# Kernel optimization log

Hardware: AMD Instinct MI355X
Metric: run time of the kernel (lower is better)

## Reference

```python
import jax, jax.numpy as jnp
import numpy as np

D_MODEL = 1024
NUM_HEADS = 16
D_HEAD = D_MODEL // NUM_HEADS
THETA = 10000.0


def _apply_rope(x, pos):
    # x: [B, H, S, Dh]; pos: [S]
    inv_freq = 1.0 / (THETA ** (jnp.arange(0, D_HEAD, 2, dtype=jnp.float32) / D_HEAD))  # [Dh/2]
    freqs = pos[:, None].astype(x.dtype) * inv_freq.astype(x.dtype)  # [S, Dh/2]
    cos = jnp.cos(freqs)  # [S, Dh/2]
    sin = jnp.sin(freqs)
    x1 = x[..., 0::2]  # [B, H, S, Dh/2]
    x2 = x[..., 1::2]
    even = x1 * cos - x2 * sin
    odd = x1 * sin + x2 * cos
    # interleave back: stack on last axis then flatten
    out = jnp.stack([even, odd], axis=-1).reshape(x.shape)
    return out


def setup_inputs() -> dict:
    key = jax.random.key(0)
    k0, k1, k2, k3, k4 = jax.random.split(key, 5)
    B, S = 2, 2048
    scale = 0.02
    return {
        "in_features": jax.random.normal(k0, (B, S, D_MODEL), dtype=jnp.float32),
        "Wq": jax.random.normal(k1, (D_MODEL, D_MODEL), dtype=jnp.float32) * scale,
        "Wk": jax.random.normal(k2, (D_MODEL, D_MODEL), dtype=jnp.float32) * scale,
        "Wv": jax.random.normal(k3, (D_MODEL, D_MODEL), dtype=jnp.float32) * scale,
        "Wo": jax.random.normal(k4, (D_MODEL, D_MODEL), dtype=jnp.float32) * scale,
    }


def reference(in_features, Wq, Wk, Wv, Wo):
    B, S, _ = in_features.shape
    H, Dh = NUM_HEADS, D_HEAD

    def proj(W):
        # torch Linear: y = x @ W^T; split heads -> [B, H, S, Dh]
        y = jnp.einsum('bsd,ed->bse', in_features, W)
        return y.reshape(B, S, H, Dh).transpose(0, 2, 1, 3)

    q = proj(Wq)
    k = proj(Wk)
    v = proj(Wv)

    pos = jnp.arange(S)
    q = _apply_rope(q, pos)
    k = _apply_rope(k, pos)

    scores = jnp.einsum('bhqd,bhkd->bhqk', q, k) / jnp.sqrt(jnp.asarray(Dh, q.dtype))
    causal = jnp.tril(jnp.ones((S, S), dtype=bool))  # True = keep
    scores = jnp.where(causal[None, None, :, :], scores, -jnp.inf)
    att = jax.nn.softmax(scores, axis=-1)
    out = jnp.einsum('bhqk,bhkd->bhqd', att, v)  # [B, H, S, Dh]
    out = out.transpose(0, 2, 1, 3).reshape(B, S, H * Dh)
    return jnp.einsum('bsd,ed->bse', out, Wo)
```

## Files before the change

kernel.cpp:

```cpp
#include <hip/hip_runtime.h>
#include <hip/hip_bf16.h>
#include <math.h>

#define D_MODEL 1024
#define NHEAD 16
#define DHEAD 64
#define SEQ 2048
#define BATCH 2
#define MTOT (BATCH * SEQ)

typedef __attribute__((ext_vector_type(8))) short bf16x8;
typedef __attribute__((ext_vector_type(4))) float f32x4;

static __device__ __forceinline__ ushort f2b(float x) {
  __hip_bfloat16 h = __float2bfloat16(x);
  union { __hip_bfloat16 h; ushort u; } cv; cv.h = h; return cv.u;
}

#define GLLDS16(gp, lp)                                                     \
  __builtin_amdgcn_global_load_lds(                                         \
      (const __attribute__((address_space(1))) unsigned int*)(gp),          \
      (__attribute__((address_space(3))) unsigned int*)(lp), 16, 0, 0)

#define QSCALE 0.18033688011112042f

__global__ __launch_bounds__(256)
void prep(const float* __restrict__ X, const float* __restrict__ Wq,
          const float* __restrict__ Wk, const float* __restrict__ Wv,
          const float* __restrict__ Wo, ushort* __restrict__ Xb,
          ushort* __restrict__ Wqb, ushort* __restrict__ Wkb,
          ushort* __restrict__ Wvb, ushort* __restrict__ Wob,
          float2* __restrict__ tbl) {
  int bid = blockIdx.x;
  if (bid >= 8192) {
    int idx = (bid - 8192) * 256 + threadIdx.x;
    int s = idx >> 5, i = idx & 31;
    float inv = exp2f((float)i * -0.4152410118609203f);
    float sn, cs;
    sincosf((float)s * inv, &sn, &cs);
    tbl[idx] = make_float2(cs, sn);
    return;
  }
  const float* in;
  ushort* out;
  int i;
  if (bid < 4096) {
    in = X; out = Xb; i = bid * 256 + threadIdx.x;
  } else {
    int ws = (bid - 4096) >> 10;
    in = (ws == 0) ? Wq : (ws == 1) ? Wk : (ws == 2) ? Wv : Wo;
    out = (ws == 0) ? Wqb : (ws == 1) ? Wkb : (ws == 2) ? Wvb : Wob;
    i = ((bid - 4096) & 1023) * 256 + threadIdx.x;
  }
  float4 v = ((const float4*)in)[i];
  ushort4 o;
  o.x = f2b(v.x); o.y = f2b(v.y); o.z = f2b(v.z); o.w = f2b(v.w);
  ((ushort4*)out)[i] = o;
}

__global__ __launch_bounds__(256)
void gemm_bf16(const ushort* __restrict__ A,
               const ushort* __restrict__ W0, const ushort* __restrict__ W1,
               const ushort* __restrict__ W2,
               const float2* __restrict__ tbl,
               float* __restrict__ outF,
               ushort* __restrict__ o0, ushort* __restrict__ o1,
               ushort* __restrict__ o2, int mode) {
  __shared__ ushort As[128 * 32];
  __shared__ ushort Bs[128 * 32];
  const int tid = threadIdx.x;
  const int lane = tid & 63;
  const int w = tid >> 6;
  const int quad = lane >> 4, l15 = lane & 15;
  const int wy = w >> 1, wx = w & 1;
  const int m0 = blockIdx.y * 128, n0 = blockIdx.x * 128;
  const int z = blockIdx.z;
  const ushort* W = (z == 0) ? W0 : (z == 1) ? W1 : W2;
  ushort* outB = (z == 0) ? o0 : (z == 1) ? o1 : o2;

  const int r0 = tid >> 2, c0 = tid & 3;
  const int gc = c0 ^ (((r0 >> 2) ^ r0) & 3);
  const ushort* Ag0 = A + (size_t)(m0 + r0) * D_MODEL + gc * 8;
  const ushort* Ag1 = A + (size_t)(m0 + r0 + 64) * D_MODEL + gc * 8;
  const ushort* Wg0 = W + (size_t)(n0 + r0) * D_MODEL + gc * 8;
  const ushort* Wg1 = W + (size_t)(n0 + r0 + 64) * D_MODEL + gc * 8;

  const int sw = (quad ^ (l15 >> 2) ^ l15) & 3;

  f32x4 acc[4][4];
#pragma unroll
  for (int i = 0; i < 4; ++i)
#pragma unroll
    for (int j = 0; j < 4; ++j) acc[i][j] = (f32x4){0.f, 0.f, 0.f, 0.f};

  for (int kt = 0; kt < D_MODEL / 32; ++kt) {
    if (kt) __syncthreads();
    GLLDS16(Ag0 + kt * 32, &As[(size_t)tid * 8]);
    GLLDS16(Ag1 + kt * 32, &As[(size_t)(tid + 256) * 8]);
    GLLDS16(Wg0 + kt * 32, &Bs[(size_t)tid * 8]);
    GLLDS16(Wg1 + kt * 32, &Bs[(size_t)(tid + 256) * 8]);
    __syncthreads();

    bf16x8 af[4], bfr[4];
#pragma unroll
    for (int mt = 0; mt < 4; ++mt) {
      int row = wy * 64 + mt * 16 + l15;
      af[mt] = *(const bf16x8*)&As[(row * 4 + sw) * 8];
    }
#pragma unroll
    for (int nt = 0; nt < 4; ++nt) {
      int row = wx * 64 + nt * 16 + l15;
      bfr[nt] = *(const bf16x8*)&Bs[(row * 4 + sw) * 8];
    }
#pragma unroll
    for (int mt = 0; mt < 4; ++mt)
#pragma unroll
      for (int nt = 0; nt < 4; ++nt)
        acc[mt][nt] = __builtin_amdgcn_mfma_f32_16x16x32_bf16(
            af[mt], bfr[nt], acc[mt][nt], 0, 0, 0);
  }

  const float qsc = (z == 0) ? QSCALE : 1.0f;
#pragma unroll
  for (int mt = 0; mt < 4; ++mt) {
    int m_base = m0 + wy * 64 + mt * 16 + quad * 4;
    int b = m_base >> 11, s_base = m_base & (SEQ - 1);
#pragma unroll
    for (int nt = 0; nt < 4; ++nt) {
      int n = n0 + wx * 64 + nt * 16 + l15;
      if (mode == 0) {
#pragma unroll
        for (int r = 0; r < 4; ++r)
          outF[(size_t)(m_base + r) * D_MODEL + n] = acc[mt][nt][r];
      } else {
        int h = n >> 6, dh = n & 63;
        if (z == 2) {
          ushort4 o;
          o.x = f2b(acc[mt][nt][0]); o.y = f2b(acc[mt][nt][1]);
          o.z = f2b(acc[mt][nt][2]); o.w = f2b(acc[mt][nt][3]);
          *(ushort4*)&outB[((size_t)(b * NHEAD + h) * DHEAD + dh) * SEQ + s_base] = o;
        } else {
          int i = nt * 8 + (l15 >> 1);
          bool evn = !(l15 & 1);
#pragma unroll
          for (int r = 0; r < 4; ++r) {
            float v = acc[mt][nt][r];
            float pv = __shfl_xor(v, 1);
            float2 csn = tbl[(s_base + r) * 32 + i];
            v = v * csn.x + (evn ? -pv * csn.y : pv * csn.y);
            v *= qsc;
            outB[(((size_t)(b * NHEAD + h)) * SEQ + s_base + r) * DHEAD + dh] = f2b(v);
          }
        }
      }
    }
  }
}

__global__ __launch_bounds__(256)
void flash_mfma(const ushort* __restrict__ Q, const ushort* __restrict__ K,
                const ushort* __restrict__ Vt, ushort* __restrict__ O) {
  __shared__ ushort Ks[64 * 64];
  __shared__ ushort Vs[64 * 64];
  __shared__ ushort Ps[4][16][68];
  const int tid = threadIdx.x;
  const int lane = tid & 63, w = tid >> 6;
  const int quad = lane >> 4, l15 = lane & 15;
  const int h = blockIdx.y, b = blockIdx.z;
  const int qt = (h >= 8) ? (31 - blockIdx.x) : blockIdx.x;
  const int bh = b * NHEAD + h;

  const ushort* Qrow = Q + ((size_t)bh * SEQ + qt * 64 + w * 16 + l15) * 64;
  bf16x8 aq0 = *(const bf16x8*)(Qrow + quad * 8);
  bf16x8 aq1 = *(const bf16x8*)(Qrow + 32 + quad * 8);

  const int rl = tid >> 3;
  const int gsc = (tid & 7) ^ (rl & 7);
  const ushort* Kg  = K  + ((size_t)bh * SEQ + rl) * 64 + gsc * 8;
  const ushort* Kg2 = Kg + (size_t)32 * 64;
  const ushort* Vg  = Vt + ((size_t)bh * 64 + rl) * SEQ + gsc * 8;
  const ushort* Vg2 = Vg + (size_t)32 * SEQ;

  const int sA = (quad ^ (l15 & 7)) * 8;
  const int sB = sA ^ 32;

  float rsl[4];
  f32x4 accO[4];
#pragma unroll
  for (int r = 0; r < 4; ++r) rsl[r] = 0.f;
#pragma unroll
  for (int nt = 0; nt < 4; ++nt) accO[nt] = (f32x4){0.f, 0.f, 0.f, 0.f};

  const int qrow0 = qt * 64 + w * 16 + quad * 4;

  for (int kt = 0; kt <= qt; ++kt) {
    __syncthreads();
    GLLDS16(Kg  + (size_t)kt * 64 * 64, &Ks[tid * 8]);
    GLLDS16(Kg2 + (size_t)kt * 64 * 64, &Ks[2048 + tid * 8]);
    GLLDS16(Vg  + kt * 64,              &Vs[tid * 8]);
    GLLDS16(Vg2 + kt * 64,              &Vs[2048 + tid * 8]);
    __syncthreads();

    f32x4 sc[4];
#pragma unroll
    for (int nt = 0; nt < 4; ++nt) {
      const ushort* kr = &Ks[(nt * 16 + l15) * 64];
      bf16x8 bk0 = *(const bf16x8*)(kr + sA);
      bf16x8 bk1 = *(const bf16x8*)(kr + sB);
      f32x4 zz = (f32x4){0.f, 0.f, 0.f, 0.f};
      zz = __builtin_amdgcn_mfma_f32_16x16x32_bf16(aq0, bk0, zz, 0, 0, 0);
      zz = __builtin_amdgcn_mfma_f32_16x16x32_bf16(aq1, bk1, zz, 0, 0, 0);
      sc[nt] = zz;
    }

    const bool diag = (kt == qt);
#pragma unroll
    for (int nt = 0; nt < 4; ++nt) {
      int kg = kt * 64 + nt * 16 + l15;
#pragma unroll
      for (int r = 0; r < 4; ++r) {
        float p = __builtin_amdgcn_exp2f(sc[nt][r]);
        if (diag && kg > qrow0 + r) p = 0.f;
        Ps[w][quad * 4 + r][nt * 16 + l15] = f2b(p);
        rsl[r] += p;
      }
    }

    bf16x8 ap0 = *(const bf16x8*)&Ps[w][l15][quad * 8];
    bf16x8 ap1 = *(const bf16x8*)&Ps[w][l15][32 + quad * 8];
#pragma unroll
    for (int nt = 0; nt < 4; ++nt) {
      const ushort* vr = &Vs[(nt * 16 + l15) * 64];
      bf16x8 bv0 = *(const bf16x8*)(vr + sA);
      bf16x8 bv1 = *(const bf16x8*)(vr + sB);
      accO[nt] = __builtin_amdgcn_mfma_f32_16x16x32_bf16(ap0, bv0, accO[nt], 0, 0, 0);
      accO[nt] = __builtin_amdgcn_mfma_f32_16x16x32_bf16(ap1, bv1, accO[nt], 0, 0, 0);
    }
  }

#pragma unroll
  for (int r = 0; r < 4; ++r) {
#pragma unroll
    for (int off = 1; off < 16; off <<= 1) rsl[r] += __shfl_xor(rsl[r], off);
  }

#pragma unroll
  for (int r = 0; r < 4; ++r) {
    float invl = 1.f / rsl[r];
    int qrow = qt * 64 + w * 16 + quad * 4 + r;
    size_t base = ((size_t)(b * SEQ + qrow)) * D_MODEL + h * 64;
#pragma unroll
    for (int nt = 0; nt < 4; ++nt)
      O[base + nt * 16 + l15] = f2b(accO[nt][r] * invl);
  }
}

extern "C" void kernel_launch(void* const* d_in, const int* in_sizes, int n_in,
                              void* d_out, int out_size, void* d_ws, size_t ws_size,
                              hipStream_t stream) {
  const float* X  = (const float*)d_in[0];
  const float* Wq = (const float*)d_in[1];
  const float* Wk = (const float*)d_in[2];
  const float* Wv = (const float*)d_in[3];
  const float* Wo = (const float*)d_in[4];
  float* out = (float*)d_out;

  ushort* Xb  = (ushort*)d_ws;
  ushort* Wqb = Xb  + (size_t)MTOT * D_MODEL;
  ushort* Wkb = Wqb + (size_t)D_MODEL * D_MODEL;
  ushort* Wvb = Wkb + (size_t)D_MODEL * D_MODEL;
  ushort* Wob = Wvb + (size_t)D_MODEL * D_MODEL;
  ushort* Qw  = Wob + (size_t)D_MODEL * D_MODEL;
  ushort* Kw  = Qw  + (size_t)MTOT * D_MODEL;
  ushort* Vtw = Kw  + (size_t)MTOT * D_MODEL;
  ushort* At  = Vtw + (size_t)MTOT * D_MODEL;
  float2* tbl = (float2*)(At + (size_t)MTOT * D_MODEL);

  prep<<<8448, 256, 0, stream>>>(X, Wq, Wk, Wv, Wo, Xb, Wqb, Wkb, Wvb, Wob, tbl);

  gemm_bf16<<<dim3(D_MODEL / 128, MTOT / 128, 3), 256, 0, stream>>>(
      Xb, Wqb, Wkb, Wvb, tbl, nullptr, Qw, Kw, Vtw, 1);

  flash_mfma<<<dim3(SEQ / 64, NHEAD, BATCH), 256, 0, stream>>>(Qw, Kw, Vtw, At);

  gemm_bf16<<<dim3(D_MODEL / 128, MTOT / 128, 1), 256, 0, stream>>>(
      At, Wob, nullptr, nullptr, tbl, out, nullptr, nullptr, nullptr, 0);
}
```

Measured before the change: 187.4 us.

## Double-buffer LDS tiles in GEMM and flash attention kernels

Both the projection GEMM and the flash attention kernel now keep two LDS buffers for their operand tiles. The first tile is prefetched before the loop, and each iteration issues the global-to-LDS loads for the next tile before computing on the current one. This is meant to hide global load latency behind MFMA work and removes one barrier per iteration. The cost is doubled LDS use per block, which may reduce occupancy. The compiler may also insert conservative waits on the async LDS loads before the LDS reads, which would cancel the intended overlap.

```diff
diff --git a/kernel.cpp b/kernel.cpp
--- a/kernel.cpp
+++ b/kernel.cpp
@@ -66,8 +66,8 @@
                float* __restrict__ outF,
                ushort* __restrict__ o0, ushort* __restrict__ o1,
                ushort* __restrict__ o2, int mode) {
-  __shared__ ushort As[128 * 32];
-  __shared__ ushort Bs[128 * 32];
+  __shared__ ushort As[2][128 * 32];
+  __shared__ ushort Bs[2][128 * 32];
   const int tid = threadIdx.x;
   const int lane = tid & 63;
   const int w = tid >> 6;
@@ -93,24 +93,31 @@
 #pragma unroll
     for (int j = 0; j < 4; ++j) acc[i][j] = (f32x4){0.f, 0.f, 0.f, 0.f};
 
+  GLLDS16(Ag0, &As[0][tid * 8]);
+  GLLDS16(Ag1, &As[0][(tid + 256) * 8]);
+  GLLDS16(Wg0, &Bs[0][tid * 8]);
+  GLLDS16(Wg1, &Bs[0][(tid + 256) * 8]);
+
   for (int kt = 0; kt < D_MODEL / 32; ++kt) {
-    if (kt) __syncthreads();
-    GLLDS16(Ag0 + kt * 32, &As[(size_t)tid * 8]);
-    GLLDS16(Ag1 + kt * 32, &As[(size_t)(tid + 256) * 8]);
-    GLLDS16(Wg0 + kt * 32, &Bs[(size_t)tid * 8]);
-    GLLDS16(Wg1 + kt * 32, &Bs[(size_t)(tid + 256) * 8]);
     __syncthreads();
+    const int cur = kt & 1, nxt = cur ^ 1;
+    if (kt + 1 < D_MODEL / 32) {
+      GLLDS16(Ag0 + (kt + 1) * 32, &As[nxt][tid * 8]);
+      GLLDS16(Ag1 + (kt + 1) * 32, &As[nxt][(tid + 256) * 8]);
+      GLLDS16(Wg0 + (kt + 1) * 32, &Bs[nxt][tid * 8]);
+      GLLDS16(Wg1 + (kt + 1) * 32, &Bs[nxt][(tid + 256) * 8]);
+    }
 
     bf16x8 af[4], bfr[4];
 #pragma unroll
     for (int mt = 0; mt < 4; ++mt) {
       int row = wy * 64 + mt * 16 + l15;
-      af[mt] = *(const bf16x8*)&As[(row * 4 + sw) * 8];
+      af[mt] = *(const bf16x8*)&As[cur][(row * 4 + sw) * 8];
     }
 #pragma unroll
     for (int nt = 0; nt < 4; ++nt) {
       int row = wx * 64 + nt * 16 + l15;
-      bfr[nt] = *(const bf16x8*)&Bs[(row * 4 + sw) * 8];
+      bfr[nt] = *(const bf16x8*)&Bs[cur][(row * 4 + sw) * 8];
     }
 #pragma unroll
     for (int mt = 0; mt < 4; ++mt)
@@ -160,8 +167,8 @@
 __global__ __launch_bounds__(256)
 void flash_mfma(const ushort* __restrict__ Q, const ushort* __restrict__ K,
                 const ushort* __restrict__ Vt, ushort* __restrict__ O) {
-  __shared__ ushort Ks[64 * 64];
-  __shared__ ushort Vs[64 * 64];
+  __shared__ ushort Ks[2][64 * 64];
+  __shared__ ushort Vs[2][64 * 64];
   __shared__ ushort Ps[4][16][68];
   const int tid = threadIdx.x;
   const int lane = tid & 63, w = tid >> 6;
@@ -193,18 +200,25 @@
 
   const int qrow0 = qt * 64 + w * 16 + quad * 4;
 
+  GLLDS16(Kg,  &Ks[0][tid * 8]);
+  GLLDS16(Kg2, &Ks[0][2048 + tid * 8]);
+  GLLDS16(Vg,  &Vs[0][tid * 8]);
+  GLLDS16(Vg2, &Vs[0][2048 + tid * 8]);
+
   for (int kt = 0; kt <= qt; ++kt) {
     __syncthreads();
-    GLLDS16(Kg  + (size_t)kt * 64 * 64, &Ks[tid * 8]);
-    GLLDS16(Kg2 + (size_t)kt * 64 * 64, &Ks[2048 + tid * 8]);
-    GLLDS16(Vg  + kt * 64,              &Vs[tid * 8]);
-    GLLDS16(Vg2 + kt * 64,              &Vs[2048 + tid * 8]);
-    __syncthreads();
+    const int cur = kt & 1, nxt = cur ^ 1;
+    if (kt < qt) {
+      GLLDS16(Kg  + (size_t)(kt + 1) * 64 * 64, &Ks[nxt][tid * 8]);
+      GLLDS16(Kg2 + (size_t)(kt + 1) * 64 * 64, &Ks[nxt][2048 + tid * 8]);
+      GLLDS16(Vg  + (kt + 1) * 64,              &Vs[nxt][tid * 8]);
+      GLLDS16(Vg2 + (kt + 1) * 64,              &Vs[nxt][2048 + tid * 8]);
+    }
 
     f32x4 sc[4];
 #pragma unroll
     for (int nt = 0; nt < 4; ++nt) {
-      const ushort* kr = &Ks[(nt * 16 + l15) * 64];
+      const ushort* kr = &Ks[cur][(nt * 16 + l15) * 64];
       bf16x8 bk0 = *(const bf16x8*)(kr + sA);
       bf16x8 bk1 = *(const bf16x8*)(kr + sB);
       f32x4 zz = (f32x4){0.f, 0.f, 0.f, 0.f};
@@ -230,7 +244,7 @@
     bf16x8 ap1 = *(const bf16x8*)&Ps[w][l15][32 + quad * 8];
 #pragma unroll
     for (int nt = 0; nt < 4; ++nt) {
-      const ushort* vr = &Vs[(nt * 16 + l15) * 64];
+      const ushort* vr = &Vs[cur][(nt * 16 + l15) * 64];
       bf16x8 bv0 = *(const bf16x8*)(vr + sA);
       bf16x8 bv1 = *(const bf16x8*)(vr + sB);
       accO[nt] = __builtin_amdgcn_mfma_f32_16x16x32_bf16(ap0, bv0, accO[nt], 0, 0, 0);
```

Measured after the change: 203.7 us. +8.7%, slower.

## Register-prefetch next K/V tile and use padded LDS instead of swizzled direct loads

Applied to the files above, without the earlier changes.

Replaces the direct global-to-LDS loads, which used an XOR swizzle, with register prefetch. The next K and V tiles are loaded into registers while the current tile is computed, then stored into padded LDS arrays (row stride 72). The goal is to overlap global memory latency with MFMA work and to avoid bank conflicts through padding rather than swizzling. In exchange it uses more VGPRs and adds extra LDS store instructions, which may lower occupancy.

```diff
diff --git a/kernel.cpp b/kernel.cpp
--- a/kernel.cpp
+++ b/kernel.cpp
@@ -160,8 +160,8 @@
 __global__ __launch_bounds__(256)
 void flash_mfma(const ushort* __restrict__ Q, const ushort* __restrict__ K,
                 const ushort* __restrict__ Vt, ushort* __restrict__ O) {
-  __shared__ ushort Ks[64 * 64];
-  __shared__ ushort Vs[64 * 64];
+  __shared__ ushort Ks[64][72];
+  __shared__ ushort Vs[64][72];
   __shared__ ushort Ps[4][16][68];
   const int tid = threadIdx.x;
   const int lane = tid & 63, w = tid >> 6;
@@ -174,15 +174,11 @@
   bf16x8 aq0 = *(const bf16x8*)(Qrow + quad * 8);
   bf16x8 aq1 = *(const bf16x8*)(Qrow + 32 + quad * 8);
 
-  const int rl = tid >> 3;
-  const int gsc = (tid & 7) ^ (rl & 7);
-  const ushort* Kg  = K  + ((size_t)bh * SEQ + rl) * 64 + gsc * 8;
-  const ushort* Kg2 = Kg + (size_t)32 * 64;
-  const ushort* Vg  = Vt + ((size_t)bh * 64 + rl) * SEQ + gsc * 8;
-  const ushort* Vg2 = Vg + (size_t)32 * SEQ;
-
-  const int sA = (quad ^ (l15 & 7)) * 8;
-  const int sB = sA ^ 32;
+  const int sr = tid >> 3, sc8 = (tid & 7) * 8;
+  const ushort* Kg0 = K + ((size_t)bh * SEQ + sr) * 64 + sc8;
+  const ushort* Kg1 = Kg0 + (size_t)32 * 64;
+  const ushort* Vg0 = Vt + ((size_t)bh * 64 + sr) * SEQ + sc8;
+  const ushort* Vg1 = Vg0 + (size_t)32 * SEQ;
 
   float rsl[4];
   f32x4 accO[4];
@@ -191,22 +187,33 @@
 #pragma unroll
   for (int nt = 0; nt < 4; ++nt) accO[nt] = (f32x4){0.f, 0.f, 0.f, 0.f};
 
+  float4 pk0 = *(const float4*)(Kg0);
+  float4 pk1 = *(const float4*)(Kg1);
+  float4 pv0 = *(const float4*)(Vg0);
+  float4 pv1 = *(const float4*)(Vg1);
+
   const int qrow0 = qt * 64 + w * 16 + quad * 4;
 
   for (int kt = 0; kt <= qt; ++kt) {
     __syncthreads();
-    GLLDS16(Kg  + (size_t)kt * 64 * 64, &Ks[tid * 8]);
-    GLLDS16(Kg2 + (size_t)kt * 64 * 64, &Ks[2048 + tid * 8]);
-    GLLDS16(Vg  + kt * 64,              &Vs[tid * 8]);
-    GLLDS16(Vg2 + kt * 64,              &Vs[2048 + tid * 8]);
+    *(float4*)&Ks[sr][sc8]      = pk0;
+    *(float4*)&Ks[sr + 32][sc8] = pk1;
+    *(float4*)&Vs[sr][sc8]      = pv0;
+    *(float4*)&Vs[sr + 32][sc8] = pv1;
     __syncthreads();
+    if (kt < qt) {
+      pk0 = *(const float4*)(Kg0 + (size_t)(kt + 1) * 64 * 64);
+      pk1 = *(const float4*)(Kg1 + (size_t)(kt + 1) * 64 * 64);
+      pv0 = *(const float4*)(Vg0 + (kt + 1) * 64);
+      pv1 = *(const float4*)(Vg1 + (kt + 1) * 64);
+    }
 
     f32x4 sc[4];
 #pragma unroll
     for (int nt = 0; nt < 4; ++nt) {
-      const ushort* kr = &Ks[(nt * 16 + l15) * 64];
-      bf16x8 bk0 = *(const bf16x8*)(kr + sA);
-      bf16x8 bk1 = *(const bf16x8*)(kr + sB);
+      const ushort* kr = &Ks[nt * 16 + l15][0];
+      bf16x8 bk0 = *(const bf16x8*)(kr + quad * 8);
+      bf16x8 bk1 = *(const bf16x8*)(kr + 32 + quad * 8);
       f32x4 zz = (f32x4){0.f, 0.f, 0.f, 0.f};
       zz = __builtin_amdgcn_mfma_f32_16x16x32_bf16(aq0, bk0, zz, 0, 0, 0);
       zz = __builtin_amdgcn_mfma_f32_16x16x32_bf16(aq1, bk1, zz, 0, 0, 0);
@@ -230,9 +237,9 @@
     bf16x8 ap1 = *(const bf16x8*)&Ps[w][l15][32 + quad * 8];
 #pragma unroll
     for (int nt = 0; nt < 4; ++nt) {
-      const ushort* vr = &Vs[(nt * 16 + l15) * 64];
-      bf16x8 bv0 = *(const bf16x8*)(vr + sA);
-      bf16x8 bv1 = *(const bf16x8*)(vr + sB);
+      const ushort* vr = &Vs[nt * 16 + l15][0];
+      bf16x8 bv0 = *(const bf16x8*)(vr + quad * 8);
+      bf16x8 bv1 = *(const bf16x8*)(vr + 32 + quad * 8);
       accO[nt] = __builtin_amdgcn_mfma_f32_16x16x32_bf16(ap0, bv0, accO[nt], 0, 0, 0);
       accO[nt] = __builtin_amdgcn_mfma_f32_16x16x32_bf16(ap1, bv1, accO[nt], 0, 0, 0);
     }
```

Measured after the change: 185.8 us. Within noise of the previous version (-0.9%).
